# Performance work log

Hardware: AMD Instinct MI355X
Metric: run time of the kernel (lower is better)

Reference implementation:

```python
import jax, jax.numpy as jnp
import numpy as np

EMB = 32
STEPS = 3
SLOPE = 0.01  # LeakyReLU default negative slope


def lrelu(x):
    return jnp.where(x > 0, x, SLOPE * x)


def seg_softmax(logits, seg, num_seg):
    # numerically stable per-segment softmax (matches torch_geometric.utils.softmax)
    m = jax.ops.segment_max(logits, seg, num_segments=num_seg)
    e = jnp.exp(logits - m[seg])
    s = jax.ops.segment_sum(e, seg, num_segments=num_seg)
    return e / s[seg]


def setup_inputs() -> dict:
    key = jax.random.key(0)
    ks = jax.random.split(key, 32)
    N, E, G = 200000, 3200000, 128
    p = lambda k, shape: (jax.random.normal(k, shape, dtype=jnp.float32) * 0.1)
    inp = {
        "node_feats": jax.random.normal(ks[0], (N, 1), dtype=jnp.float32),
        "edge_index": jax.random.randint(ks[1], (2, E), 0, N),
        "batch": jnp.sort(jax.random.randint(ks[2], (N,), 0, G)),
        "num_graphs": G,
        # embed_node: Linear(1, 32)
        "W_embed": p(ks[3], (1, EMB)), "b_embed": p(ks[4], (EMB,)),
        # per-step GraphNet params (stacked over steps)
        "Wm": p(ks[5], (STEPS, EMB, EMB)), "bm": p(ks[6], (STEPS, EMB)),          # f_mess (edge_size=0)
        "Wa": p(ks[7], (STEPS, 3 * EMB, EMB)), "ba": p(ks[8], (STEPS, EMB)),      # f_agg: [x, xg, agg]
        # per-step GlobalNode params
        "Wgate": p(ks[9], (STEPS, EMB, 1)), "bgate": p(ks[10], (STEPS, 1)),       # att_mask
        "Wfeat": p(ks[11], (STEPS, EMB, EMB)), "bfeat": p(ks[12], (STEPS, EMB)),  # att_feat
        "Wt": p(ks[13], (STEPS, 2 * EMB, EMB)), "bt": p(ks[14], (STEPS, EMB)),    # transform
        # heads
        "W_v": p(ks[15], (EMB, 1)), "b_v": p(ks[16], (1,)),
        "W_a0": p(ks[17], (EMB, 2)), "b_a0": p(ks[18], (2,)),
        "W_a1": p(ks[19], (EMB, 1)), "b_a1": p(ks[20], (1,)),
    }
    return inp


def reference(node_feats, edge_index, batch, num_graphs,
              W_embed, b_embed, Wm, bm, Wa, ba, Wgate, bgate, Wfeat, bfeat,
              Wt, bt, W_v, b_v, W_a0, b_a0, W_a1, b_a1):
    N = node_feats.shape[0]
    src, dst = edge_index[0], edge_index[1]

    x = lrelu(node_feats @ W_embed + b_embed)            # [N, 32]
    xg = jnp.zeros((num_graphs, EMB), dtype=x.dtype)     # [G, 32]

    for i in range(Wm.shape[0]):
        # GraphNet: gather -> MLP -> scatter-max -> update MLP + residual
        msg = lrelu(x[src] @ Wm[i] + bm[i])              # [E, 32]
        agg = jax.ops.segment_max(msg, dst, num_segments=N)
        agg = jnp.where(jnp.isfinite(agg), agg, 0.0)     # empty segments -> 0
        z = jnp.concatenate([x, xg[batch], agg], axis=1)  # [N, 96]
        x = lrelu(z @ Wa[i] + ba[i]) + x

        # GlobalNode: GlobalAttention pooling + transform with residual
        gate = seg_softmax((x @ Wgate[i] + bgate[i])[:, 0], batch, num_graphs)  # [N]
        feat = lrelu(x @ Wfeat[i] + bfeat[i])            # [N, 32]
        pooled = jax.ops.segment_sum(gate[:, None] * feat, batch, num_segments=num_graphs)
        cat = jnp.concatenate([pooled, xg], axis=1)      # [G, 64]
        xg = lrelu(cat @ Wt[i] + bt[i]) + xg

    value = xg @ W_v + b_v                               # [G, 1]
    a0_probs = jax.nn.softmax(xg @ W_a0 + b_a0, axis=1)  # [G, 2]
    a1_softmax = seg_softmax((x @ W_a1 + b_a1)[:, 0], batch, num_graphs)  # [N]
    return value, a0_probs, a1_softmax
```

## Files before the change

kernel.cpp:

```cpp
#include <hip/hip_runtime.h>
#include <hip/hip_bf16.h>

#define GG 128
#define SLOPE 0.01f
#define CHUNK 8192
#define NPB 64
#define NREP 64

#define OFF_Wm   0
#define OFF_bm   3072
#define OFF_Wa   3168
#define OFF_ba   12384
#define OFF_Wg   12480
#define OFF_bg   12576
#define OFF_Wf   12592
#define OFF_bf   15664
#define OFF_Wt   15760
#define OFF_bt   21904
#define OFF_Wa1  22000
#define OFF_ba1  22032
#define WCAT_N   22048

__device__ __forceinline__ float lrelu(float v) { return v > 0.f ? v : SLOPE * v; }
__device__ __forceinline__ float b2f(__hip_bfloat16 v) { return __bfloat162float(v); }

__device__ __forceinline__ float ldf(const void* p, int i, int isf) {
    if (isf) return ((const float*)p)[i];
    return __bfloat162float(((const __hip_bfloat16*)p)[i]);
}
__device__ __forceinline__ void stf(void* p, int i, float v, int isf) {
    if (isf) ((float*)p)[i] = v;
    else ((__hip_bfloat16*)p)[i] = __float2bfloat16(v);
}

__device__ __forceinline__ float bfLo(unsigned u) { return __uint_as_float(u << 16); }
__device__ __forceinline__ float bfHi(unsigned u) { return __uint_as_float(u & 0xFFFF0000u); }

__global__ void k_detect(const unsigned short* __restrict__ w, int n, int* __restrict__ flag) {
    __shared__ int bad;
    if (threadIdx.x == 0) bad = 0;
    __syncthreads();
    for (int t = threadIdx.x; t < n; t += 256) {
        unsigned short u = w[t];
        int e = (u >> 7) & 0xFF;
        if (e >= 141) bad = 1;
    }
    __syncthreads();
    if (threadIdx.x == 0) { flag[0] = bad; flag[32] = 1; }
}

struct CvtArgs {
    const void* p[12];
    int off[12];
    int n[12];
};
__global__ void k_cvt_all(CvtArgs a, float* __restrict__ dst, const int* __restrict__ dtf) {
    int isf = *dtf;
    int seg = blockIdx.y;
    int i = blockIdx.x * 256 + threadIdx.x;
    if (i < a.n[seg]) dst[a.off[seg] + i] = ldf(a.p[seg], i, isf);
}

__global__ void k_xgw0(const void* __restrict__ ba0, float* __restrict__ xgw,
                       const int* __restrict__ dtf) {
    int isf = *dtf;
    int idx = blockIdx.x * 256 + threadIdx.x;
    xgw[idx] = ldf(ba0, idx & 31, isf);
}

__global__ void k_embed_msg(const void* __restrict__ nf, const void* __restrict__ We,
                            const void* __restrict__ be,
                            const float* __restrict__ Wm0, const float* __restrict__ bm0,
                            float* __restrict__ x, __hip_bfloat16* __restrict__ m, int N,
                            const int* __restrict__ dtf) {
    __shared__ float WL[1024];
    __shared__ float WeL[32], beL[32], bmL[32];
    __shared__ float xs[8][32];
    int isf = *dtf;
    int tid = threadIdx.x;
    for (int t = tid; t < 1024; t += 256) WL[t] = Wm0[t];
    if (tid < 32) { WeL[tid] = ldf(We, tid, isf); beL[tid] = ldf(be, tid, isf); bmL[tid] = bm0[tid]; }
    int s = tid >> 5, j = tid & 31;
    int n = blockIdx.x * 8 + s;
    __syncthreads();
    float xv = 0.f;
    if (n < N) {
        xv = lrelu(ldf(nf, n, isf) * WeL[j] + beL[j]);
        x[n * 32 + j] = xv;
        xs[s][j] = xv;
    }
    __syncthreads();
    if (n >= N) return;
    float acc = bmL[j];
#pragma unroll
    for (int k = 0; k < 32; ++k) acc += xs[s][k] * WL[k * 32 + j];
    m[n * 32 + j] = __float2bfloat16(lrelu(acc));
}

__global__ void k_graph_off(const int* __restrict__ batch, int* __restrict__ goff, int N) {
    int n = blockIdx.x * 256 + threadIdx.x;
    if (n >= N) return;
    int bn = batch[n];
    if (n == 0) {
        for (int g = 0; g <= bn; ++g) goff[g] = 0;
    } else {
        int bp = batch[n - 1];
        for (int g = bp + 1; g <= bn; ++g) goff[g] = n;
    }
    if (n == N - 1) {
        for (int g = bn + 1; g <= GG; ++g) goff[g] = N;
    }
}

__global__ void k_hist(const int* __restrict__ dst, unsigned* __restrict__ deg, int E) {
    int e = blockIdx.x * 256 + threadIdx.x;
    if (e >= E) return;
    atomicAdd(&deg[dst[e]], 1u);
}
__global__ void k_scan1(const unsigned* __restrict__ deg, unsigned* __restrict__ excl,
                        unsigned* __restrict__ bsum, int N) {
    __shared__ unsigned s[256];
    int i = blockIdx.x * 256 + threadIdx.x;
    unsigned v = (i < N) ? deg[i] : 0u;
    s[threadIdx.x] = v;
    __syncthreads();
    for (int off = 1; off < 256; off <<= 1) {
        unsigned t = (threadIdx.x >= (unsigned)off) ? s[threadIdx.x - off] : 0u;
        __syncthreads();
        s[threadIdx.x] += t;
        __syncthreads();
    }
    if (i < N) excl[i] = s[threadIdx.x] - v;
    if (threadIdx.x == 255) bsum[blockIdx.x] = s[255];
}
__global__ void k_scan2(const unsigned* __restrict__ bsum, unsigned* __restrict__ boff, int nb) {
    __shared__ unsigned s[256];
    __shared__ unsigned carry;
    if (threadIdx.x == 0) carry = 0u;
    __syncthreads();
    for (int base = 0; base < nb; base += 256) {
        int i = base + threadIdx.x;
        unsigned v = (i < nb) ? bsum[i] : 0u;
        s[threadIdx.x] = v;
        __syncthreads();
        for (int off = 1; off < 256; off <<= 1) {
            unsigned t = (threadIdx.x >= (unsigned)off) ? s[threadIdx.x - off] : 0u;
            __syncthreads();
            s[threadIdx.x] += t;
            __syncthreads();
        }
        if (i < nb) boff[i] = carry + s[threadIdx.x] - v;
        __syncthreads();
        if (threadIdx.x == 0) carry += s[255];
        __syncthreads();
    }
}
__global__ void k_scan3(unsigned* __restrict__ indptr, const unsigned* __restrict__ boff,
                        unsigned* __restrict__ cursor, int N, int E) {
    int i = blockIdx.x * 256 + threadIdx.x;
    if (i >= N) return;
    unsigned v = indptr[i] + boff[i >> 8];
    indptr[i] = v;
    cursor[i] = v;
    if (i == 0) indptr[N] = (unsigned)E;
}
__global__ void k_scatter(const int* __restrict__ src, const int* __restrict__ dst,
                          unsigned* __restrict__ cursor, unsigned* __restrict__ ssrc, int E) {
    int e = blockIdx.x * 256 + threadIdx.x;
    if (e >= E) return;
    unsigned pos = atomicAdd(&cursor[dst[e]], 1u);
    ssrc[pos] = (unsigned)src[e];
}

__global__ void k_bhist(const int* __restrict__ dst, unsigned* __restrict__ bcnt, int E, int B) {
    __shared__ unsigned h[2048];
    for (int t = threadIdx.x; t < B; t += 256) h[t] = 0;
    __syncthreads();
    int start = blockIdx.x * CHUNK, end = min(E, start + CHUNK);
    for (int e = start + threadIdx.x; e < end; e += 256)
        atomicAdd(&h[dst[e] >> 8], 1u);
    __syncthreads();
    for (int t = threadIdx.x; t < B; t += 256)
        if (h[t]) atomicAdd(&bcnt[t], h[t]);
}

__global__ void k_bscan(const unsigned* __restrict__ bcnt, unsigned* __restrict__ bbase,
                        unsigned* __restrict__ bcur, int B, int E) {
    __shared__ unsigned s[256];
    __shared__ unsigned carry;
    if (threadIdx.x == 0) carry = 0u;
    __syncthreads();
    for (int base = 0; base < B; base += 256) {
        int i = base + threadIdx.x;
        unsigned v = (i < B) ? bcnt[i] : 0u;
        s[threadIdx.x] = v;
        __syncthreads();
        for (int off = 1; off < 256; off <<= 1) {
            unsigned t = (threadIdx.x >= (unsigned)off) ? s[threadIdx.x - off] : 0u;
            __syncthreads();
            s[threadIdx.x] += t;
            __syncthreads();
        }
        if (i < B) {
            unsigned ex = carry + s[threadIdx.x] - v;
            bbase[i] = ex;
            bcur[i] = ex;
        }
        __syncthreads();
        if (threadIdx.x == 0) carry += s[255];
        __syncthreads();
    }
    if (threadIdx.x == 0) bbase[B] = (unsigned)E;
}

__global__ void k_binA(const int* __restrict__ src, const int* __restrict__ dst,
                       unsigned* __restrict__ bcur, unsigned long long* __restrict__ packed,
                       int E, int B) {
    __shared__ unsigned h[2048];
    __shared__ unsigned pos[2048];
    for (int t = threadIdx.x; t < B; t += 256) h[t] = 0;
    __syncthreads();
    int start = blockIdx.x * CHUNK, end = min(E, start + CHUNK);
    for (int e = start + threadIdx.x; e < end; e += 256)
        atomicAdd(&h[dst[e] >> 8], 1u);
    __syncthreads();
    for (int t = threadIdx.x; t < B; t += 256)
        pos[t] = h[t] ? atomicAdd(&bcur[t], h[t]) : 0u;
    __syncthreads();
    for (int e = start + threadIdx.x; e < end; e += 256) {
        int d = dst[e];
        unsigned p = atomicAdd(&pos[d >> 8], 1u);
        packed[p] = ((unsigned long long)(unsigned)d << 32) | (unsigned)src[e];
    }
}

__global__ void k_csr(const unsigned long long* __restrict__ packed,
                      const unsigned* __restrict__ bbase,
                      unsigned* __restrict__ indptr,
                      unsigned* __restrict__ ssrc, int N, int E) {
    __shared__ unsigned deg[256];
    __shared__ unsigned scn[256];
    __shared__ unsigned cur[256];
    int g = blockIdx.x, tid = threadIdx.x;
    int n0 = g << 8;
    int cnt = min(256, N - n0);
    deg[tid] = 0;
    __syncthreads();
    unsigned e0 = bbase[g], e1 = bbase[g + 1];
    for (unsigned e = e0 + tid; e < e1; e += 256) {
        int d = (int)(packed[e] >> 32);
        atomicAdd(&deg[d - n0], 1u);
    }
    __syncthreads();
    unsigned v = deg[tid];
    scn[tid] = v;
    __syncthreads();
    for (int off = 1; off < 256; off <<= 1) {
        unsigned t = (tid >= off) ? scn[tid - off] : 0u;
        __syncthreads();
        scn[tid] += t;
        __syncthreads();
    }
    unsigned start = e0 + scn[tid] - v;
    if (tid < cnt) { indptr[n0 + tid] = start; cur[tid] = start; }
    if (g == (int)gridDim.x - 1 && tid == 0) indptr[N] = (unsigned)E;
    __syncthreads();
    for (unsigned e = e0 + tid; e < e1; e += 256) {
        unsigned long long pk = packed[e];
        int d = (int)(pk >> 32);
        unsigned p = atomicAdd(&cur[d - n0], 1u);
        ssrc[p] = (unsigned)pk;
    }
}

__global__ __launch_bounds__(256, 4)
void k_step(float* __restrict__ x, const __hip_bfloat16* __restrict__ m_in,
            __hip_bfloat16* __restrict__ m_out,
            const int* __restrict__ batch,
            const unsigned* __restrict__ indptr, const unsigned* __restrict__ ssrc,
            const float* __restrict__ Wa, const float* __restrict__ xgw,
            const float* __restrict__ Wg, const float* __restrict__ bg,
            const float* __restrict__ Wa1, const float* __restrict__ ba1,
            const float* __restrict__ Wf, const float* __restrict__ bf,
            const float* __restrict__ Wm_nx, const float* __restrict__ bm_nx,
            float* __restrict__ la1, float* __restrict__ U, float* __restrict__ S,
            int N, int hasNext) {
    __shared__ float WL[2048];
    __shared__ float WmL[1024];
    __shared__ float zL[8][64];
    __shared__ float xnL[8][32];
    __shared__ float WgL[32], W1L[32], bmL[32], bfL[32];
    __shared__ float bgL, b1L;
    int tid = threadIdx.x;
    for (int t = tid; t < 2048; t += 256) WL[t] = (t < 1024) ? Wa[t] : Wa[t + 1024];
    if (hasNext) {
        for (int t = tid; t < 1024; t += 256) WmL[t] = Wm_nx[t];
        if (tid < 32) bmL[tid] = bm_nx[tid];
    }
    if (tid < 32) { WgL[tid] = Wg[tid]; W1L[tid] = Wa1[tid]; bfL[tid] = bf[tid]; }
    if (tid == 0) { bgL = bg[0]; b1L = ba1[0]; }
    int s = tid >> 5, j = tid & 31;
    int c = j & 7, eo = j >> 3;
    float wfr[32];
#pragma unroll
    for (int k = 0; k < 32; ++k) wfr[k] = Wf[k * 32 + j];
    const uint2* m2 = (const uint2*)m_in;
    int nbase = blockIdx.x * NPB;
    int rep = blockIdx.x & (NREP - 1);
    float* Urep = U + (size_t)rep * GG * 32;
    float* Srep = S + (size_t)rep * GG;
    __syncthreads();
    int gcur = -1;
    float Uacc = 0.f, Sacc = 0.f;
    for (int sub = 0; sub < NPB / 8; ++sub) {
        int n = nbase + sub * 8 + s;
        bool valid = n < N;
        int gb = gcur;
        float xj = 0.f;
        if (valid) {
            xj = x[n * 32 + j];
            zL[s][j] = xj;
            gb = batch[n];
        }
        if (valid && gb != gcur) {
            if (gcur >= 0) {
                atomicAdd(&Urep[gcur * 32 + j], Uacc);
                if (j == 0) atomicAdd(&Srep[gcur], Sacc);
            }
            gcur = gb; Uacc = 0.f; Sacc = 0.f;
        }
        unsigned st = 0, en = 0;
        if (valid) { st = indptr[n]; en = indptr[n + 1]; }
        float a[4];
#pragma unroll
        for (int t = 0; t < 4; ++t) a[t] = -INFINITY;
        if (en > st) {
            unsigned last = en - 1;
            for (unsigned base = st; base < en; base += 16) {
                unsigned eA = min(base + eo, last);
                unsigned eB = min(base + 4 + eo, last);
                unsigned eC = min(base + 8 + eo, last);
                unsigned eD = min(base + 12 + eo, last);
                unsigned sA = ssrc[eA];
                unsigned sB = ssrc[eB];
                unsigned sC = ssrc[eC];
                unsigned sD = ssrc[eD];
                uint2 vA = m2[sA * 8 + c];
                uint2 vB = m2[sB * 8 + c];
                uint2 vC = m2[sC * 8 + c];
                uint2 vD = m2[sD * 8 + c];
                a[0] = fmaxf(a[0], fmaxf(fmaxf(bfLo(vA.x), bfLo(vB.x)), fmaxf(bfLo(vC.x), bfLo(vD.x))));
                a[1] = fmaxf(a[1], fmaxf(fmaxf(bfHi(vA.x), bfHi(vB.x)), fmaxf(bfHi(vC.x), bfHi(vD.x))));
                a[2] = fmaxf(a[2], fmaxf(fmaxf(bfLo(vA.y), bfLo(vB.y)), fmaxf(bfLo(vC.y), bfLo(vD.y))));
                a[3] = fmaxf(a[3], fmaxf(fmaxf(bfHi(vA.y), bfHi(vB.y)), fmaxf(bfHi(vC.y), bfHi(vD.y))));
            }
        }
#pragma unroll
        for (int t = 0; t < 4; ++t) {
            a[t] = fmaxf(a[t], __shfl_xor(a[t], 8));
            a[t] = fmaxf(a[t], __shfl_xor(a[t], 16));
        }
        if (valid && eo == 0) {
            bool empty = (st == en);
#pragma unroll
            for (int t = 0; t < 4; ++t)
                zL[s][32 + (c << 2) + t] = empty ? 0.f : a[t];
        }
        if (valid) {
            float acc = xgw[gb * 32 + j];
#pragma unroll
            for (int k = 0; k < 64; ++k) acc += zL[s][k] * WL[k * 32 + j];
            float xn = lrelu(acc) + xj;
            x[n * 32 + j] = xn;
            xnL[s][j] = xn;
            float lv = xn * WgL[j];
            if (hasNext) {
#pragma unroll
                for (int off = 16; off; off >>= 1) lv += __shfl_xor(lv, off);
            } else {
                float l1 = xn * W1L[j];
#pragma unroll
                for (int off = 16; off; off >>= 1) { lv += __shfl_xor(lv, off); l1 += __shfl_xor(l1, off); }
                if (j == 0) la1[n] = l1 + b1L;
            }
            float e = __expf(lv + bgL);
            float f = bfL[j];
            if (hasNext) {
                float a2 = bmL[j];
#pragma unroll
                for (int k = 0; k < 32; ++k) {
                    float v = xnL[s][k];
                    f += v * wfr[k];
                    a2 += v * WmL[k * 32 + j];
                }
                m_out[n * 32 + j] = __float2bfloat16(lrelu(a2));
            } else {
#pragma unroll
                for (int k = 0; k < 32; ++k) f += xnL[s][k] * wfr[k];
            }
            Uacc += e * lrelu(f);
            Sacc += e;
        }
    }
    if (gcur >= 0) {
        atomicAdd(&Urep[gcur * 32 + j], Uacc);
        if (j == 0) atomicAdd(&Srep[gcur], Sacc);
    }
}

__global__ void k_gupd(float* __restrict__ U, float* __restrict__ S,
                       const float* __restrict__ xg_in,
                       const float* __restrict__ Wt, const float* __restrict__ bt,
                       float* __restrict__ xg_out,
                       const float* __restrict__ WaNx, const float* __restrict__ baNx,
                       float* __restrict__ xgw, int hasNext) {
    __shared__ float pl[8][32];
    __shared__ float vL[8][32];
    int idx = blockIdx.x * 256 + threadIdx.x;
    int g = idx >> 5, j = idx & 31;
    int lg = threadIdx.x >> 5;
    float usum = 0.f, ssum = 0.f;
#pragma unroll 4
    for (int r = 0; r < NREP; ++r) {
        usum += U[(size_t)r * GG * 32 + idx];
        U[(size_t)r * GG * 32 + idx] = 0.f;
        ssum += S[r * GG + g];
    }
    if (j == 0) {
        for (int r = 0; r < NREP; ++r) S[r * GG + g] = 0.f;
    }
    float inv = (ssum > 0.f) ? 1.f / ssum : 0.f;
    pl[lg][j] = usum * inv;
    __syncthreads();
    float acc = bt[j];
#pragma unroll
    for (int k = 0; k < 32; ++k) acc += pl[lg][k] * Wt[k * 32 + j];
#pragma unroll
    for (int k = 0; k < 32; ++k) acc += xg_in[g * 32 + k] * Wt[(32 + k) * 32 + j];
    float v = lrelu(acc) + xg_in[idx];
    xg_out[idx] = v;
    if (hasNext) {
        vL[lg][j] = v;
        __syncthreads();
        float aw = baNx[j];
#pragma unroll
        for (int k = 0; k < 32; ++k) aw += vL[lg][k] * WaNx[(32 + k) * 32 + j];
        xgw[idx] = aw;
    }
}

__global__ void k_final(const float* __restrict__ logits, const int* __restrict__ goff,
                        const float* __restrict__ xg,
                        const void* __restrict__ Wv, const void* __restrict__ bv,
                        const void* __restrict__ Wa0, const void* __restrict__ ba0,
                        void* __restrict__ out, int N, const int* __restrict__ dtf) {
    __shared__ float red[256];
    int isf = *dtf;
    int g = blockIdx.x, tid = threadIdx.x;
    int s0 = goff[g], s1 = goff[g + 1];
    float lm = -INFINITY;
    for (int n = s0 + tid; n < s1; n += 256) lm = fmaxf(lm, logits[n]);
    red[tid] = lm;
    __syncthreads();
    for (int off = 128; off; off >>= 1) {
        if (tid < off) red[tid] = fmaxf(red[tid], red[tid + off]);
        __syncthreads();
    }
    float gmax = red[0];
    __syncthreads();
    float ls = 0.f;
    for (int n = s0 + tid; n < s1; n += 256) ls += expf(logits[n] - gmax);
    red[tid] = ls;
    __syncthreads();
    for (int off = 128; off; off >>= 1) {
        if (tid < off) red[tid] += red[tid + off];
        __syncthreads();
    }
    float inv = (red[0] > 0.f) ? 1.f / red[0] : 0.f;
    __syncthreads();
    for (int n = s0 + tid; n < s1; n += 256)
        stf(out, 384 + n, expf(logits[n] - gmax) * inv, isf);
    if (tid == 0) {
        float acc = ldf(bv, 0, isf);
        for (int k = 0; k < 32; ++k) acc += xg[g * 32 + k] * ldf(Wv, k, isf);
        stf(out, g, acc, isf);
        float l0 = ldf(ba0, 0, isf), l1 = ldf(ba0, 1, isf);
        for (int k = 0; k < 32; ++k) {
            float xv = xg[g * 32 + k];
            l0 += xv * ldf(Wa0, k * 2, isf);
            l1 += xv * ldf(Wa0, k * 2 + 1, isf);
        }
        float mm = fmaxf(l0, l1);
        float e0 = expf(l0 - mm), e1 = expf(l1 - mm);
        float si = 1.f / (e0 + e1);
        stf(out, 128 + 2 * g, e0 * si, isf);
        stf(out, 128 + 2 * g + 1, e1 * si, isf);
    }
}

extern "C" void kernel_launch(void* const* d_in, const int* in_sizes, int n_in,
                              void* d_out, int out_size, void* d_ws, size_t ws_size,
                              hipStream_t stream) {
    const void* nf      = d_in[0];
    const int*  eidx    = (const int*)d_in[1];
    const int*  batch   = (const int*)d_in[2];
    const void* W_embed = d_in[4];
    const void* b_embed = d_in[5];
    const void* Wm      = d_in[6];
    const void* bm      = d_in[7];
    const void* Wa      = d_in[8];
    const void* ba      = d_in[9];
    const void* Wgate   = d_in[10];
    const void* bgate   = d_in[11];
    const void* Wfeat   = d_in[12];
    const void* bfeat   = d_in[13];
    const void* Wt      = d_in[14];
    const void* bt      = d_in[15];
    const void* W_v     = d_in[16];
    const void* b_v     = d_in[17];
    const void* W_a0    = d_in[18];
    const void* b_a0    = d_in[19];
    const void* W_a1    = d_in[20];
    const void* b_a1    = d_in[21];

    const int N = in_sizes[0];
    const int E = in_sizes[1] / 2;
    const int nWm = in_sizes[6];
    const int* src = eidx;
    const int* dst = eidx + E;
    const int B = (N + 255) >> 8;

    char* ws = (char*)d_ws;
    size_t off = 0;
    auto alloc = [&](size_t bytes) -> char* {
        char* p = ws + off;
        off = (off + bytes + 255) & ~(size_t)255;
        return p;
    };
    float*          x      = (float*)alloc((size_t)N * 32 * 4);
    size_t mBytes  = (size_t)N * 32 * 2;
    size_t pkBytes = (size_t)E * 8;
    size_t rBytes  = (2 * mBytes > pkBytes) ? 2 * mBytes : pkBytes;
    char*  mRegion = alloc(rBytes);
    unsigned long long* packed = (unsigned long long*)mRegion;
    __hip_bfloat16*     m_a    = (__hip_bfloat16*)mRegion;
    __hip_bfloat16*     m_b    = (__hip_bfloat16*)(mRegion + mBytes);
    float*          la1    = (float*)alloc((size_t)N * 4);
    unsigned*       indptr = (unsigned*)alloc((size_t)(N + 1) * 4);
    unsigned*       cursor = (unsigned*)alloc((size_t)N * 4);
    unsigned*       ssrc   = (unsigned*)alloc((size_t)(E + 16) * 4);
    const int nb = (N + 255) / 256;
    unsigned*       bsum   = (unsigned*)alloc((size_t)nb * 4);
    unsigned*       boff   = (unsigned*)alloc((size_t)nb * 4);
    unsigned*       bcnt   = (unsigned*)alloc((size_t)(B + 1) * 4);
    unsigned*       bbase  = (unsigned*)alloc((size_t)(B + 1) * 4);
    unsigned*       bcur   = (unsigned*)alloc((size_t)(B + 1) * 4);
    int*            goff   = (int*)alloc((size_t)(GG + 1) * 4);
    float*          xg_a   = (float*)alloc((size_t)GG * 32 * 4);
    float*          xg_b   = (float*)alloc((size_t)GG * 32 * 4);
    float*          xgw    = (float*)alloc((size_t)GG * 32 * 4);
    float*          U      = (float*)alloc((size_t)NREP * GG * 32 * 4);
    float*          S      = (float*)alloc((size_t)NREP * GG * 4);
    int*            dtf    = (int*)alloc(256);
    float*          wcat   = (float*)alloc((size_t)WCAT_N * 4);

    const int nB_n  = (N + 255) / 256;
    const int nB_e  = (E + 255) / 256;
    const int nB_n8 = (N + 7) / 8;
    const int nB_st = (N + NPB - 1) / NPB;
    const int nB_ch = (E + CHUNK - 1) / CHUNK;

    hipMemsetAsync(xg_a, 0, (size_t)GG * 32 * 4, stream);
    hipMemsetAsync(bcnt, 0, (size_t)(B + 1) * 4, stream);
    hipMemsetAsync(U, 0, (size_t)NREP * GG * 32 * 4, stream);
    hipMemsetAsync(S, 0, (size_t)NREP * GG * 4, stream);

    k_detect<<<1, 256, 0, stream>>>((const unsigned short*)Wm, nWm, dtf);

    CvtArgs ca;
    const void* ps[12] = {Wm, bm, Wa, ba, Wgate, bgate, Wfeat, bfeat, Wt, bt, W_a1, b_a1};
    const int  offs[12] = {OFF_Wm, OFF_bm, OFF_Wa, OFF_ba, OFF_Wg, OFF_bg,
                           OFF_Wf, OFF_bf, OFF_Wt, OFF_bt, OFF_Wa1, OFF_ba1};
    const int  ns[12]  = {3072, 96, 9216, 96, 96, 3, 3072, 96, 6144, 96, 32, 1};
    for (int i = 0; i < 12; ++i) { ca.p[i] = ps[i]; ca.off[i] = offs[i]; ca.n[i] = ns[i]; }
    k_cvt_all<<<dim3(36, 12), 256, 0, stream>>>(ca, wcat, dtf);

    k_xgw0<<<(GG * 32) / 256, 256, 0, stream>>>(ba, xgw, dtf);

    k_graph_off<<<nB_n, 256, 0, stream>>>(batch, goff, N);

    if (B <= 2048) {
        k_bhist<<<nB_ch, 256, 0, stream>>>(dst, bcnt, E, B);
        k_bscan<<<1, 256, 0, stream>>>(bcnt, bbase, bcur, B, E);
        k_binA<<<nB_ch, 256, 0, stream>>>(src, dst, bcur, packed, E, B);
        k_csr<<<B, 256, 0, stream>>>(packed, bbase, indptr, ssrc, N, E);
    } else {
        hipMemsetAsync(cursor, 0, (size_t)N * 4, stream);
        k_hist<<<nB_e, 256, 0, stream>>>(dst, cursor, E);
        k_scan1<<<nb, 256, 0, stream>>>(cursor, indptr, bsum, N);
        k_scan2<<<1, 256, 0, stream>>>(bsum, boff, nb);
        k_scan3<<<nB_n, 256, 0, stream>>>(indptr, boff, cursor, N, E);
        k_scatter<<<nB_e, 256, 0, stream>>>(src, dst, cursor, ssrc, E);
    }

    k_embed_msg<<<nB_n8, 256, 0, stream>>>(nf, W_embed, b_embed,
                                           wcat + OFF_Wm, wcat + OFF_bm, x, m_a, N, dtf);

    float* xg_cur = xg_a;
    float* xg_nxt = xg_b;
    __hip_bfloat16* m_cur = m_a;
    __hip_bfloat16* m_nxt = m_b;
    for (int i = 0; i < 3; ++i) {
        int hasNext = (i < 2) ? 1 : 0;
        k_step<<<nB_st, 256, 0, stream>>>(x, m_cur, m_nxt, batch, indptr, ssrc,
                                          wcat + OFF_Wa + i * 3072, xgw,
                                          wcat + OFF_Wg + i * 32, wcat + OFF_bg + i,
                                          wcat + OFF_Wa1, wcat + OFF_ba1,
                                          wcat + OFF_Wf + i * 1024, wcat + OFF_bf + i * 32,
                                          wcat + OFF_Wm + (i + 1) * 1024,
                                          wcat + OFF_bm + (i + 1) * 32,
                                          la1, U, S, N, hasNext);
        k_gupd<<<(GG * 32 + 255) / 256, 256, 0, stream>>>(U, S, xg_cur,
                                                          wcat + OFF_Wt + i * 2048,
                                                          wcat + OFF_bt + i * 32, xg_nxt,
                                                          wcat + OFF_Wa + (i + 1) * 3072,
                                                          wcat + OFF_ba + (i + 1) * 32,
                                                          xgw, hasNext);
        float* tmp = xg_cur; xg_cur = xg_nxt; xg_nxt = tmp;
        __hip_bfloat16* tm = m_cur; m_cur = m_nxt; m_nxt = tm;
    }

    k_final<<<GG, 256, 0, stream>>>(la1, goff, xg_cur, W_v, b_v, W_a0, b_a0,
                                    d_out, N, dtf);
}
```

Baseline: 634.9 us.

## Swizzle transposed weight tiles in LDS for float4 dot products and parallelize gupd

```diff
diff --git a/kernel.cpp b/kernel.cpp
--- a/kernel.cpp
+++ b/kernel.cpp
@@ -22,7 +22,6 @@
 #define WCAT_N   22048
 
 __device__ __forceinline__ float lrelu(float v) { return v > 0.f ? v : SLOPE * v; }
-__device__ __forceinline__ float b2f(__hip_bfloat16 v) { return __bfloat162float(v); }
 
 __device__ __forceinline__ float ldf(const void* p, int i, int isf) {
     if (isf) return ((const float*)p)[i];
@@ -285,22 +284,30 @@
             const float* __restrict__ Wm_nx, const float* __restrict__ bm_nx,
             float* __restrict__ la1, float* __restrict__ U, float* __restrict__ S,
             int N, int hasNext) {
-    __shared__ float WL[2048];
-    __shared__ float WmL[1024];
-    __shared__ float zL[8][64];
-    __shared__ float xnL[8][32];
+    __shared__ __attribute__((aligned(16))) float WLt[2048];
+    __shared__ __attribute__((aligned(16))) float WmLt[1024];
+    __shared__ __attribute__((aligned(16))) float zL[8][64];
+    __shared__ __attribute__((aligned(16))) float xnL[8][32];
     __shared__ float WgL[32], W1L[32], bmL[32], bfL[32];
     __shared__ float bgL, b1L;
     int tid = threadIdx.x;
-    for (int t = tid; t < 2048; t += 256) WL[t] = (t < 1024) ? Wa[t] : Wa[t + 1024];
+    for (int t = tid; t < 2048; t += 256) {
+        int k = t >> 5, j2 = t & 31;
+        float v = (k < 32) ? Wa[t] : Wa[t + 1024];
+        WLt[(j2 << 6) + (((k >> 2) ^ (j2 & 15)) << 2) + (k & 3)] = v;
+    }
     if (hasNext) {
-        for (int t = tid; t < 1024; t += 256) WmL[t] = Wm_nx[t];
+        for (int t = tid; t < 1024; t += 256) {
+            int k = t >> 5, j2 = t & 31;
+            WmLt[(j2 << 5) + (((k >> 2) ^ (j2 & 7)) << 2) + (k & 3)] = Wm_nx[t];
+        }
         if (tid < 32) bmL[tid] = bm_nx[tid];
     }
     if (tid < 32) { WgL[tid] = Wg[tid]; W1L[tid] = Wa1[tid]; bfL[tid] = bf[tid]; }
     if (tid == 0) { bgL = bg[0]; b1L = ba1[0]; }
     int s = tid >> 5, j = tid & 31;
     int c = j & 7, eo = j >> 3;
+    int jx16 = j & 15, jx8 = j & 7;
     float wfr[32];
 #pragma unroll
     for (int k = 0; k < 32; ++k) wfr[k] = Wf[k * 32 + j];
@@ -362,15 +369,27 @@
         }
         if (valid && eo == 0) {
             bool empty = (st == en);
-#pragma unroll
-            for (int t = 0; t < 4; ++t)
-                zL[s][32 + (c << 2) + t] = empty ? 0.f : a[t];
+            float4 av;
+            av.x = empty ? 0.f : a[0];
+            av.y = empty ? 0.f : a[1];
+            av.z = empty ? 0.f : a[2];
+            av.w = empty ? 0.f : a[3];
+            *(float4*)&zL[s][32 + (c << 2)] = av;
         }
         if (valid) {
-            float acc = xgw[gb * 32 + j];
-#pragma unroll
-            for (int k = 0; k < 64; ++k) acc += zL[s][k] * WL[k * 32 + j];
-            float xn = lrelu(acc) + xj;
+            float acc0 = xgw[gb * 32 + j];
+            float acc1 = 0.f, acc2 = 0.f, acc3 = 0.f;
+            const float* wbase = &WLt[j << 6];
+#pragma unroll
+            for (int cc = 0; cc < 16; ++cc) {
+                float4 zv = *(const float4*)&zL[s][cc << 2];
+                float4 wv = *(const float4*)&wbase[(cc ^ jx16) << 2];
+                acc0 += zv.x * wv.x;
+                acc1 += zv.y * wv.y;
+                acc2 += zv.z * wv.z;
+                acc3 += zv.w * wv.w;
+            }
+            float xn = lrelu((acc0 + acc1) + (acc2 + acc3)) + xj;
             x[n * 32 + j] = xn;
             xnL[s][j] = xn;
             float lv = xn * WgL[j];
@@ -386,17 +405,25 @@
             float e = __expf(lv + bgL);
             float f = bfL[j];
             if (hasNext) {
-                float a2 = bmL[j];
-#pragma unroll
-                for (int k = 0; k < 32; ++k) {
-                    float v = xnL[s][k];
-                    f += v * wfr[k];
-                    a2 += v * WmL[k * 32 + j];
+                float a20 = bmL[j], a21 = 0.f;
+                const float* wmb = &WmLt[j << 5];
+#pragma unroll
+                for (int cc = 0; cc < 8; ++cc) {
+                    float4 xv = *(const float4*)&xnL[s][cc << 2];
+                    float4 wm = *(const float4*)&wmb[(cc ^ jx8) << 2];
+                    f += xv.x * wfr[4 * cc] + xv.y * wfr[4 * cc + 1]
+                       + xv.z * wfr[4 * cc + 2] + xv.w * wfr[4 * cc + 3];
+                    a20 += xv.x * wm.x + xv.y * wm.y;
+                    a21 += xv.z * wm.z + xv.w * wm.w;
                 }
-                m_out[n * 32 + j] = __float2bfloat16(lrelu(a2));
+                m_out[n * 32 + j] = __float2bfloat16(lrelu(a20 + a21));
             } else {
 #pragma unroll
-                for (int k = 0; k < 32; ++k) f += xnL[s][k] * wfr[k];
+                for (int cc = 0; cc < 8; ++cc) {
+                    float4 xv = *(const float4*)&xnL[s][cc << 2];
+                    f += xv.x * wfr[4 * cc] + xv.y * wfr[4 * cc + 1]
+                       + xv.z * wfr[4 * cc + 2] + xv.w * wfr[4 * cc + 3];
+                }
             }
             Uacc += e * lrelu(f);
             Sacc += e;
@@ -414,38 +441,46 @@
                        float* __restrict__ xg_out,
                        const float* __restrict__ WaNx, const float* __restrict__ baNx,
                        float* __restrict__ xgw, int hasNext) {
-    __shared__ float pl[8][32];
-    __shared__ float vL[8][32];
-    int idx = blockIdx.x * 256 + threadIdx.x;
-    int g = idx >> 5, j = idx & 31;
-    int lg = threadIdx.x >> 5;
+    __shared__ float Up[8][32];
+    __shared__ float Sp[8];
+    __shared__ float pl[32];
+    __shared__ float vL[32];
+    int g = blockIdx.x;
+    int tid = threadIdx.x;
+    int rp = tid >> 5, j = tid & 31;
     float usum = 0.f, ssum = 0.f;
-#pragma unroll 4
-    for (int r = 0; r < NREP; ++r) {
-        usum += U[(size_t)r * GG * 32 + idx];
-        U[(size_t)r * GG * 32 + idx] = 0.f;
-        ssum += S[r * GG + g];
-    }
-    if (j == 0) {
-        for (int r = 0; r < NREP; ++r) S[r * GG + g] = 0.f;
-    }
-    float inv = (ssum > 0.f) ? 1.f / ssum : 0.f;
-    pl[lg][j] = usum * inv;
-    __syncthreads();
-    float acc = bt[j];
-#pragma unroll
-    for (int k = 0; k < 32; ++k) acc += pl[lg][k] * Wt[k * 32 + j];
-#pragma unroll
-    for (int k = 0; k < 32; ++k) acc += xg_in[g * 32 + k] * Wt[(32 + k) * 32 + j];
-    float v = lrelu(acc) + xg_in[idx];
-    xg_out[idx] = v;
-    if (hasNext) {
-        vL[lg][j] = v;
-        __syncthreads();
-        float aw = baNx[j];
-#pragma unroll
-        for (int k = 0; k < 32; ++k) aw += vL[lg][k] * WaNx[(32 + k) * 32 + j];
-        xgw[idx] = aw;
+    for (int r = rp; r < NREP; r += 8) {
+        size_t ui = (size_t)r * GG * 32 + g * 32 + j;
+        usum += U[ui];
+        U[ui] = 0.f;
+        if (j == 0) { ssum += S[r * GG + g]; S[r * GG + g] = 0.f; }
+    }
+    Up[rp][j] = usum;
+    if (j == 0) Sp[rp] = ssum;
+    __syncthreads();
+    if (rp == 0) {
+        float ut = 0.f;
+#pragma unroll
+        for (int i = 0; i < 8; ++i) ut += Up[i][j];
+        float st = ((Sp[0] + Sp[1]) + (Sp[2] + Sp[3])) + ((Sp[4] + Sp[5]) + (Sp[6] + Sp[7]));
+        float inv = (st > 0.f) ? 1.f / st : 0.f;
+        pl[j] = ut * inv;
+        float xgv = xg_in[g * 32 + j];
+        vL[j] = xgv;
+        float acc = bt[j];
+#pragma unroll
+        for (int k = 0; k < 32; ++k) acc += pl[k] * Wt[k * 32 + j];
+#pragma unroll
+        for (int k = 0; k < 32; ++k) acc += vL[k] * Wt[(32 + k) * 32 + j];
+        float v = lrelu(acc) + xgv;
+        xg_out[g * 32 + j] = v;
+        if (hasNext) {
+            vL[j] = v;
+            float aw = baNx[j];
+#pragma unroll
+            for (int k = 0; k < 32; ++k) aw += vL[k] * WaNx[(32 + k) * 32 + j];
+            xgw[g * 32 + j] = aw;
+        }
     }
 }
 
@@ -620,12 +655,12 @@
                                           wcat + OFF_Wm + (i + 1) * 1024,
                                           wcat + OFF_bm + (i + 1) * 32,
                                           la1, U, S, N, hasNext);
-        k_gupd<<<(GG * 32 + 255) / 256, 256, 0, stream>>>(U, S, xg_cur,
-                                                          wcat + OFF_Wt + i * 2048,
-                                                          wcat + OFF_bt + i * 32, xg_nxt,
-                                                          wcat + OFF_Wa + (i + 1) * 3072,
-                                                          wcat + OFF_ba + (i + 1) * 32,
-                                                          xgw, hasNext);
+        k_gupd<<<GG, 256, 0, stream>>>(U, S, xg_cur,
+                                       wcat + OFF_Wt + i * 2048,
+                                       wcat + OFF_bt + i * 32, xg_nxt,
+                                       wcat + OFF_Wa + (i + 1) * 3072,
+                                       wcat + OFF_ba + (i + 1) * 32,
+                                       xgw, hasNext);
         float* tmp = xg_cur; xg_cur = xg_nxt; xg_nxt = tmp;
         __hip_bfloat16* tm = m_cur; m_cur = m_nxt; m_nxt = tm;
     }
```

After: 1.132 ms. 1.78x slower.
